# Performance work log

Measured on AMD Instinct MI355X. Metric: run time of the kernel, lower is better.

## Reference

```python
import jax, jax.numpy as jnp
import numpy as np

N_NODES = 50000
N_EDGES = 800000
N_GRAPHS = 64
D_IN = 96
D_HID = 96
D_OUT = 2
NEG_SLOPE = 0.2


def setup_inputs() -> dict:
    key = jax.random.key(0)
    ks = jax.random.split(key, 9)
    x = jax.random.normal(ks[0], (N_NODES, D_IN), dtype=jnp.float32)
    edge_index = jax.random.randint(ks[1], (2, N_EDGES), 0, N_NODES, dtype=jnp.int32)
    batch = jnp.sort(jax.random.randint(ks[2], (N_NODES,), 0, N_GRAPHS, dtype=jnp.int32))
    s1 = 1.0 / np.sqrt(D_IN)
    s2 = 1.0 / np.sqrt(D_HID)
    W1 = jax.random.normal(ks[3], (D_IN, D_HID), dtype=jnp.float32) * s1
    b1 = jnp.zeros((D_HID,), dtype=jnp.float32)
    W2 = jax.random.normal(ks[4], (D_HID, D_HID), dtype=jnp.float32) * s2
    b2 = jnp.zeros((D_HID,), dtype=jnp.float32)
    Wc = jax.random.normal(ks[5], (D_HID, D_OUT), dtype=jnp.float32) * s2
    bc = jnp.zeros((D_OUT,), dtype=jnp.float32)
    return {"x": x, "edge_index": edge_index, "batch": batch,
            "W1": W1, "b1": b1, "W2": W2, "b2": b2, "Wc": Wc, "bc": bc}


def _gcn_conv(h, W, b, src, dst, n_nodes):
    # GCNConv (Kipf): add self-loops, symmetric deg^-1/2 normalization.
    hW = h @ W  # [N, F]
    deg = jnp.zeros((n_nodes,), dtype=hW.dtype).at[dst].add(1.0) + 1.0  # +1 self-loop
    dinv = jax.lax.rsqrt(deg)
    coef = (dinv[src] * dinv[dst])[:, None]            # [E, 1]
    agg = jnp.zeros_like(hW).at[dst].add(hW[src] * coef)
    out = agg + hW * (dinv * dinv)[:, None] + b        # self-loop term: deg^-1 * hW
    return out


def _leaky(h):
    return jnp.where(h > 0, h, NEG_SLOPE * h)


def reference(x, edge_index, batch, W1, b1, W2, b2, Wc, bc):
    src, dst = edge_index[0], edge_index[1]
    h = _leaky(_gcn_conv(x, W1, b1, src, dst, N_NODES))
    h = _leaky(_gcn_conv(h, W2, b2, src, dst, N_NODES))
    # global_mean_pool over graph ids
    sums = jax.ops.segment_sum(h, batch, num_segments=N_GRAPHS)
    cnts = jax.ops.segment_sum(jnp.ones((N_NODES,), dtype=h.dtype), batch, num_segments=N_GRAPHS)
    pooled = sums / jnp.maximum(cnts, 1.0)[:, None]    # [G, F]
    return pooled @ Wc + bc                             # [G, D_OUT]
```

## Files before the change

kernel.cpp:

```cpp
#include <hip/hip_runtime.h>
#include <hip/hip_fp16.h>

#define NN 50000
#define NE 800000
#define NG 64
#define DF 96
#define SLOPE 0.2f
#define NBK 196
#define EB 196
#define PC 12

using half8 = __attribute__((ext_vector_type(8))) _Float16;
using f32x4 = __attribute__((ext_vector_type(4))) float;

__global__ __launch_bounds__(256) void k_hist(const int* __restrict__ dst,
                                              int* __restrict__ hist2d) {
  __shared__ int h[NBK];
  int t = threadIdx.x;
  if (t < NBK) h[t] = 0;
  __syncthreads();
  int base = blockIdx.x * 4096;
  for (int k = 0; k < 16; ++k) {
    int e = base + k * 256 + t;
    if (e < NE) atomicAdd(&h[dst[e] >> 8], 1);
  }
  __syncthreads();
  if (t < NBK) hist2d[blockIdx.x * NBK + t] = h[t];
}

__global__ __launch_bounds__(256) void k_colscan(const int* __restrict__ hist2d,
                                                 int* __restrict__ colpref,
                                                 int* __restrict__ coltotal,
                                                 const int* __restrict__ batch,
                                                 int* __restrict__ gstart) {
  __shared__ int s[256];
  int col = blockIdx.x;
  int b = threadIdx.x;
  int v = (b < EB) ? hist2d[b * NBK + col] : 0;
  s[b] = v;
  __syncthreads();
  for (int o = 1; o < 256; o <<= 1) {
    int u = (b >= o) ? s[b - o] : 0;
    __syncthreads();
    s[b] += u;
    __syncthreads();
  }
  if (b < EB) colpref[b * NBK + col] = s[b] - v;
  if (b == 255) coltotal[col] = s[b];
  if (blockIdx.x == 0 && b <= NG) {
    int g = b, lo = 0, hi = NN;
    while (lo < hi) {
      int mid = (lo + hi) >> 1;
      if (batch[mid] < g) lo = mid + 1; else hi = mid;
    }
    gstart[g] = lo;
  }
}

__global__ __launch_bounds__(256) void k_bin2(const int* __restrict__ src,
                                              const int* __restrict__ dst,
                                              const int* __restrict__ hist2d,
                                              const int* __restrict__ coltotal,
                                              const int* __restrict__ colpref,
                                              int* __restrict__ binned) {
  __shared__ int h[NBK], loff[NBK], cur[NBK], gb[NBK];
  __shared__ int tmp[256];
  __shared__ int stage[4096];
  __shared__ unsigned char sbk[4096];
  int t = threadIdx.x;
  int ctv = (t < NBK) ? coltotal[t] : 0;
  tmp[t] = ctv;
  __syncthreads();
  for (int o = 1; o < 256; o <<= 1) {
    int u = (t >= o) ? tmp[t - o] : 0;
    __syncthreads();
    tmp[t] += u;
    __syncthreads();
  }
  int bbase_t = tmp[t] - ctv;
  if (t < NBK) h[t] = hist2d[blockIdx.x * NBK + t];
  __syncthreads();
  tmp[t] = (t < NBK) ? h[t] : 0;
  __syncthreads();
  for (int o = 1; o < 256; o <<= 1) {
    int u = (t >= o) ? tmp[t - o] : 0;
    __syncthreads();
    tmp[t] += u;
    __syncthreads();
  }
  if (t < NBK) {
    int excl = tmp[t] - h[t];
    loff[t] = excl;
    cur[t] = excl;
    gb[t] = bbase_t + colpref[blockIdx.x * NBK + t];
  }
  __syncthreads();
  int base = blockIdx.x * 4096;
  for (int k = 0; k < 16; ++k) {
    int e = base + k * 256 + t;
    if (e < NE) {
      int d = dst[e];
      int b = d >> 8;
      int p = atomicAdd(&cur[b], 1);
      stage[p] = src[e] | ((d & 255) << 16);
      sbk[p] = (unsigned char)b;
    }
  }
  __syncthreads();
  int tot = min(4096, NE - base);
  for (int i = t; i < tot; i += 256) {
    int b = sbk[i];
    binned[gb[b] + (i - loff[b])] = stage[i];
  }
}

__global__ __launch_bounds__(256) void k_csr(const int* __restrict__ binned,
                                             const int* __restrict__ coltotal,
                                             float* __restrict__ dinv,
                                             int* __restrict__ row_start,
                                             unsigned short* __restrict__ csr_src) {
  __shared__ int h[256], cur[256], tmp[256];
  int t = threadIdx.x;
  int b = blockIdx.x;
  int ctv = (t < NBK) ? coltotal[t] : 0;
  h[t] = ctv;
  tmp[t] = ctv;
  __syncthreads();
  for (int o = 1; o < 256; o <<= 1) {
    int u = (t >= o) ? tmp[t - o] : 0;
    __syncthreads();
    tmp[t] += u;
    __syncthreads();
  }
  int ebeg = tmp[b] - h[b];
  int eend = tmp[b];
  __syncthreads();
  h[t] = 0;
  __syncthreads();
  for (int i = ebeg + t; i < eend; i += 256) atomicAdd(&h[(unsigned)binned[i] >> 16], 1);
  __syncthreads();
  tmp[t] = h[t];
  __syncthreads();
  for (int o = 1; o < 256; o <<= 1) {
    int v = (t >= o) ? tmp[t - o] : 0;
    __syncthreads();
    tmp[t] += v;
    __syncthreads();
  }
  int excl = tmp[t] - h[t];
  int rs = ebeg + excl;
  cur[t] = rs;
  int n = b * 256 + t;
  if (n < NN) {
    row_start[n] = rs;
    dinv[n] = rsqrtf((float)h[t] + 1.0f);
  }
  if (b == NBK - 1 && t == 255) row_start[NN] = NE;
  __syncthreads();
  for (int i = ebeg + t; i < eend; i += 256) {
    int pr = binned[i];
    int p = atomicAdd(&cur[(unsigned)pr >> 16], 1);
    csr_src[p] = (unsigned short)(pr & 0xFFFF);
  }
}

#define WTP 104
template <typename T>
__global__ __launch_bounds__(256) void k_gemm(const T* __restrict__ X,
                                              const float* __restrict__ W,
                                              const float* __restrict__ dinv,
                                              __half* __restrict__ G) {
  __shared__ alignas(16) _Float16 Wt[DF * WTP];
  int t = threadIdx.x;
  for (int i = t; i < DF * DF; i += 256) {
    int k = i / DF, c = i % DF;
    Wt[c * WTP + k] = (_Float16)W[i];
  }
  __syncthreads();

  int wave = t >> 6;
  int lane = t & 63;
  int lrow = lane & 15;
  int kgrp = lane >> 4;
  int rowbase = blockIdx.x * 64 + wave * 16;
  int arow = min(rowbase + lrow, NN - 1);

  half8 a[3];
#pragma unroll
  for (int kt = 0; kt < 3; ++kt) {
    int k0 = kt * 32 + kgrp * 8;
    if constexpr (sizeof(T) == 4) {
      const float4* xp = (const float4*)((const float*)X + (size_t)arow * DF + k0);
      float4 v0 = xp[0], v1 = xp[1];
      a[kt][0] = (_Float16)v0.x; a[kt][1] = (_Float16)v0.y;
      a[kt][2] = (_Float16)v0.z; a[kt][3] = (_Float16)v0.w;
      a[kt][4] = (_Float16)v1.x; a[kt][5] = (_Float16)v1.y;
      a[kt][6] = (_Float16)v1.z; a[kt][7] = (_Float16)v1.w;
    } else {
      a[kt] = *(const half8*)((const _Float16*)X + (size_t)arow * DF + k0);
    }
  }

  float dvv[4];
  int orow0 = rowbase + kgrp * 4;
#pragma unroll
  for (int r = 0; r < 4; ++r)
    dvv[r] = (orow0 + r < NN) ? dinv[orow0 + r] : 0.f;

#pragma unroll
  for (int ct = 0; ct < 6; ++ct) {
    int colbase = ct * 16;
    f32x4 acc = {0.f, 0.f, 0.f, 0.f};
#pragma unroll
    for (int kt = 0; kt < 3; ++kt) {
      half8 b = *(const half8*)&Wt[(colbase + lrow) * WTP + kt * 32 + kgrp * 8];
      acc = __builtin_amdgcn_mfma_f32_16x16x32_f16(a[kt], b, acc, 0, 0, 0);
    }
#pragma unroll
    for (int r = 0; r < 4; ++r) {
      int orow = orow0 + r;
      if (orow < NN)
        G[(size_t)orow * DF + colbase + lrow] = __float2half(acc[r] * dvv[r]);
    }
  }
}

__global__ __launch_bounds__(256) void k_agg(const __half* __restrict__ G,
                                             const float* __restrict__ dinv,
                                             const float* __restrict__ bias,
                                             const int* __restrict__ row_start,
                                             const unsigned short* __restrict__ csr_src,
                                             __half* __restrict__ H) {
  int lane = threadIdx.x & 15;
  int n = blockIdx.x * 16 + (threadIdx.x >> 4);
  if (n >= NN) return;
  const unsigned* rn = (const unsigned*)(G + (size_t)n * DF);
  unsigned su0 = rn[lane], su1 = rn[lane + 16], su2 = rn[lane + 32];
  float2 f0 = __half22float2(*(__half2*)&su0);
  float2 f1 = __half22float2(*(__half2*)&su1);
  float2 f2 = __half22float2(*(__half2*)&su2);
  float a00 = f0.x, a01 = f0.y, a10 = f1.x, a11 = f1.y, a20 = f2.x, a21 = f2.y;

  int s = row_start[n], e = row_start[n + 1];
  for (int j0 = s; j0 < e; j0 += 16) {
    int my = (j0 + lane < e) ? (int)csr_src[j0 + lane] : 0;
    int cnt = min(16, e - j0);
    int jj = 0;
    for (; jj + 8 <= cnt; jj += 8) {
      unsigned u[8][3];
#pragma unroll
      for (int q = 0; q < 8; ++q) {
        int srcn = __shfl(my, jj + q, 16);
        const unsigned* r2 = (const unsigned*)(G + (size_t)srcn * DF);
        u[q][0] = r2[lane];
        u[q][1] = r2[lane + 16];
        u[q][2] = r2[lane + 32];
      }
#pragma unroll
      for (int q = 0; q < 8; ++q) {
        float2 g0 = __half22float2(*(__half2*)&u[q][0]);
        float2 g1 = __half22float2(*(__half2*)&u[q][1]);
        float2 g2 = __half22float2(*(__half2*)&u[q][2]);
        a00 += g0.x; a01 += g0.y;
        a10 += g1.x; a11 += g1.y;
        a20 += g2.x; a21 += g2.y;
      }
    }
    for (; jj < cnt; ++jj) {
      int srcn = __shfl(my, jj, 16);
      const unsigned* r2 = (const unsigned*)(G + (size_t)srcn * DF);
      unsigned v0 = r2[lane], v1 = r2[lane + 16], v2 = r2[lane + 32];
      float2 g0 = __half22float2(*(__half2*)&v0);
      float2 g1 = __half22float2(*(__half2*)&v1);
      float2 g2 = __half22float2(*(__half2*)&v2);
      a00 += g0.x; a01 += g0.y;
      a10 += g1.x; a11 += g1.y;
      a20 += g2.x; a21 += g2.y;
    }
  }
  float dv = dinv[n];
  float2 b0 = *(const float2*)(bias + 2 * lane);
  float2 b1 = *(const float2*)(bias + 2 * lane + 32);
  float2 b2 = *(const float2*)(bias + 2 * lane + 64);
  float v00 = dv * a00 + b0.x, v01 = dv * a01 + b0.y;
  float v10 = dv * a10 + b1.x, v11 = dv * a11 + b1.y;
  float v20 = dv * a20 + b2.x, v21 = dv * a21 + b2.y;
  v00 = v00 > 0.f ? v00 : SLOPE * v00;
  v01 = v01 > 0.f ? v01 : SLOPE * v01;
  v10 = v10 > 0.f ? v10 : SLOPE * v10;
  v11 = v11 > 0.f ? v11 : SLOPE * v11;
  v20 = v20 > 0.f ? v20 : SLOPE * v20;
  v21 = v21 > 0.f ? v21 : SLOPE * v21;
  __half2* hp = (__half2*)(H + (size_t)n * DF);
  hp[lane] = __floats2half2_rn(v00, v01);
  hp[lane + 16] = __floats2half2_rn(v10, v11);
  hp[lane + 32] = __floats2half2_rn(v20, v21);
}

__global__ __launch_bounds__(384) void k_pool2(const __half* __restrict__ H,
                                               const int* __restrict__ gstart,
                                               float* __restrict__ partial) {
  int g = blockIdx.x / PC, c = blockIdx.x % PC;
  int f2 = threadIdx.x % 48;
  int r = threadIdx.x / 48;
  int s = gstart[g], e = gstart[g + 1];
  int len = (e - s + PC - 1) / PC;
  int cs = s + c * len, ce = min(cs + len, e);
  float ax = 0.f, ay = 0.f;
  for (int n = cs + r; n < ce; n += 8) {
    float2 v = __half22float2(((const __half2*)(H + (size_t)n * DF))[f2]);
    ax += v.x;
    ay += v.y;
  }
  __shared__ float2 red[8][48];
  red[r][f2] = float2{ax, ay};
  __syncthreads();
  if (r == 0) {
    float sx = 0.f, sy = 0.f;
#pragma unroll
    for (int q = 0; q < 8; ++q) { sx += red[q][f2].x; sy += red[q][f2].y; }
    partial[(size_t)blockIdx.x * DF + 2 * f2] = sx;
    partial[(size_t)blockIdx.x * DF + 2 * f2 + 1] = sy;
  }
}

__global__ __launch_bounds__(128) void k_pool3(const float* __restrict__ partial,
                                               const int* __restrict__ gstart,
                                               const float* __restrict__ Wc,
                                               const float* __restrict__ bc,
                                               float* __restrict__ out) {
  __shared__ float pm[DF];
  int g = blockIdx.x;
  int t = threadIdx.x;
  if (t < DF) {
    float s = 0.f;
    for (int c = 0; c < PC; ++c) s += partial[(size_t)(g * PC + c) * DF + t];
    float cnt = (float)(gstart[g + 1] - gstart[g]);
    pm[t] = s / fmaxf(cnt, 1.0f);
  }
  __syncthreads();
  if (t < 2) {
    float s = 0.f;
    for (int c = 0; c < DF; ++c) s += pm[c] * Wc[c * 2 + t];
    out[g * 2 + t] = s + bc[t];
  }
}

extern "C" void kernel_launch(void* const* d_in, const int* in_sizes, int n_in,
                              void* d_out, int out_size, void* d_ws, size_t ws_size,
                              hipStream_t stream) {
  const float* x = (const float*)d_in[0];
  const int* ei = (const int*)d_in[1];
  const int* batch = (const int*)d_in[2];
  const float* W1 = (const float*)d_in[3];
  const float* b1 = (const float*)d_in[4];
  const float* W2 = (const float*)d_in[5];
  const float* b2 = (const float*)d_in[6];
  const float* Wc = (const float*)d_in[7];
  const float* bc = (const float*)d_in[8];
  float* out = (float*)d_out;
  const int* srcv = ei;
  const int* dstv = ei + NE;

  char* p = (char*)d_ws;
  auto alloc = [&](size_t bytes) {
    char* r = p;
    p += (bytes + 255) & ~(size_t)255;
    return r;
  };
  int* hist2d = (int*)alloc((size_t)EB * NBK * sizeof(int));
  int* colpref = (int*)alloc((size_t)EB * NBK * sizeof(int));
  int* coltotal = (int*)alloc((size_t)NBK * sizeof(int));
  int* gstart = (int*)alloc((size_t)(NG + 1) * sizeof(int));
  int* row_start = (int*)alloc((size_t)(NN + 1) * sizeof(int));
  int* binned = (int*)alloc((size_t)NE * sizeof(int));
  unsigned short* csr_src = (unsigned short*)alloc((size_t)NE * sizeof(unsigned short));
  float* dinv = (float*)alloc((size_t)NN * sizeof(float));
  __half* g = (__half*)alloc((size_t)NN * DF * sizeof(__half));
  __half* h = (__half*)alloc((size_t)NN * DF * sizeof(__half));
  float* partial = (float*)alloc((size_t)NG * PC * DF * sizeof(float));

  k_hist<<<EB, 256, 0, stream>>>(dstv, hist2d);
  k_colscan<<<NBK, 256, 0, stream>>>(hist2d, colpref, coltotal, batch, gstart);
  k_bin2<<<EB, 256, 0, stream>>>(srcv, dstv, hist2d, coltotal, colpref, binned);
  k_csr<<<NBK, 256, 0, stream>>>(binned, coltotal, dinv, row_start, csr_src);

  const int GB = (NN + 63) / 64;
  k_gemm<float><<<GB, 256, 0, stream>>>(x, W1, dinv, g);
  k_agg<<<(NN + 15) / 16, 256, 0, stream>>>(g, dinv, b1, row_start, csr_src, h);
  k_gemm<__half><<<GB, 256, 0, stream>>>((const __half*)h, W2, dinv, g);
  k_agg<<<(NN + 15) / 16, 256, 0, stream>>>(g, dinv, b2, row_start, csr_src, h);

  k_pool2<<<NG * PC, 384, 0, stream>>>(h, gstart, partial);
  k_pool3<<<NG, 128, 0, stream>>>(partial, gstart, Wc, bc, out);
}
```

Baseline: 126.1 us.

## Fuse CSR build into one cooperative kernel and pool inside final aggregation

Merges the four graph-preprocessing kernels (histogram, column scan, binning, CSR build) into a single cooperative kernel that uses grid-wide syncs between phases, cutting launch gaps. The second aggregation kernel now reduces its 16 node rows per block into per-graph sums in shared memory and atomically adds them to the partial buffer. This removes the write of the final hidden features and the separate pooling pass. It relies on all 196 blocks being co-resident for the cooperative launch. It also introduces float atomics, which make the summation order nondeterministic.

```diff
diff --git a/kernel.cpp b/kernel.cpp
--- a/kernel.cpp
+++ b/kernel.cpp
@@ -1,5 +1,8 @@
 #include <hip/hip_runtime.h>
 #include <hip/hip_fp16.h>
+#include <hip/hip_cooperative_groups.h>
+
+namespace cg = cooperative_groups;
 
 #define NN 50000
 #define NE 800000
@@ -8,159 +11,154 @@
 #define SLOPE 0.2f
 #define NBK 196
 #define EB 196
-#define PC 12
 
 using half8 = __attribute__((ext_vector_type(8))) _Float16;
 using f32x4 = __attribute__((ext_vector_type(4))) float;
 
-__global__ __launch_bounds__(256) void k_hist(const int* __restrict__ dst,
-                                              int* __restrict__ hist2d) {
-  __shared__ int h[NBK];
+__global__ __launch_bounds__(256) void k_build(const int* __restrict__ src,
+                                               const int* __restrict__ dst,
+                                               const int* __restrict__ batch,
+                                               int* __restrict__ hist2d,
+                                               int* __restrict__ colpref,
+                                               int* __restrict__ coltotal,
+                                               int* __restrict__ gstart,
+                                               int* __restrict__ binned,
+                                               float* __restrict__ dinv,
+                                               int* __restrict__ row_start,
+                                               unsigned short* __restrict__ csr_src,
+                                               float* __restrict__ partial) {
+  cg::grid_group grid = cg::this_grid();
+  __shared__ int h[256], cur[256], tmp[256];
+  __shared__ int loff[NBK], gb[NBK];
+  __shared__ int stage[4096];
+  __shared__ unsigned char sbk[4096];
   int t = threadIdx.x;
+  int blk = blockIdx.x;
+
   if (t < NBK) h[t] = 0;
   __syncthreads();
-  int base = blockIdx.x * 4096;
+  int base = blk * 4096;
   for (int k = 0; k < 16; ++k) {
     int e = base + k * 256 + t;
     if (e < NE) atomicAdd(&h[dst[e] >> 8], 1);
   }
   __syncthreads();
-  if (t < NBK) hist2d[blockIdx.x * NBK + t] = h[t];
-}
-
-__global__ __launch_bounds__(256) void k_colscan(const int* __restrict__ hist2d,
-                                                 int* __restrict__ colpref,
-                                                 int* __restrict__ coltotal,
-                                                 const int* __restrict__ batch,
-                                                 int* __restrict__ gstart) {
-  __shared__ int s[256];
-  int col = blockIdx.x;
-  int b = threadIdx.x;
-  int v = (b < EB) ? hist2d[b * NBK + col] : 0;
-  s[b] = v;
-  __syncthreads();
-  for (int o = 1; o < 256; o <<= 1) {
-    int u = (b >= o) ? s[b - o] : 0;
-    __syncthreads();
-    s[b] += u;
-    __syncthreads();
-  }
-  if (b < EB) colpref[b * NBK + col] = s[b] - v;
-  if (b == 255) coltotal[col] = s[b];
-  if (blockIdx.x == 0 && b <= NG) {
-    int g = b, lo = 0, hi = NN;
-    while (lo < hi) {
-      int mid = (lo + hi) >> 1;
-      if (batch[mid] < g) lo = mid + 1; else hi = mid;
-    }
-    gstart[g] = lo;
-  }
-}
-
-__global__ __launch_bounds__(256) void k_bin2(const int* __restrict__ src,
-                                              const int* __restrict__ dst,
-                                              const int* __restrict__ hist2d,
-                                              const int* __restrict__ coltotal,
-                                              const int* __restrict__ colpref,
-                                              int* __restrict__ binned) {
-  __shared__ int h[NBK], loff[NBK], cur[NBK], gb[NBK];
-  __shared__ int tmp[256];
-  __shared__ int stage[4096];
-  __shared__ unsigned char sbk[4096];
-  int t = threadIdx.x;
-  int ctv = (t < NBK) ? coltotal[t] : 0;
-  tmp[t] = ctv;
-  __syncthreads();
-  for (int o = 1; o < 256; o <<= 1) {
-    int u = (t >= o) ? tmp[t - o] : 0;
-    __syncthreads();
-    tmp[t] += u;
-    __syncthreads();
-  }
-  int bbase_t = tmp[t] - ctv;
-  if (t < NBK) h[t] = hist2d[blockIdx.x * NBK + t];
-  __syncthreads();
-  tmp[t] = (t < NBK) ? h[t] : 0;
-  __syncthreads();
-  for (int o = 1; o < 256; o <<= 1) {
-    int u = (t >= o) ? tmp[t - o] : 0;
-    __syncthreads();
-    tmp[t] += u;
-    __syncthreads();
-  }
-  if (t < NBK) {
+  if (t < NBK) hist2d[blk * NBK + t] = h[t];
+  grid.sync();
+
+  {
+    int col = blk;
+    int v = (t < EB) ? hist2d[t * NBK + col] : 0;
+    tmp[t] = v;
+    __syncthreads();
+    for (int o = 1; o < 256; o <<= 1) {
+      int u = (t >= o) ? tmp[t - o] : 0;
+      __syncthreads();
+      tmp[t] += u;
+      __syncthreads();
+    }
+    if (t < EB) colpref[t * NBK + col] = tmp[t] - v;
+    if (t == 255) coltotal[col] = tmp[t];
+    if (blk == 0 && t <= NG) {
+      int g = t, lo = 0, hi = NN;
+      while (lo < hi) {
+        int mid = (lo + hi) >> 1;
+        if (batch[mid] < g) lo = mid + 1; else hi = mid;
+      }
+      gstart[g] = lo;
+    }
+    if (blk == 1)
+      for (int i = t; i < NG * DF; i += 256) partial[i] = 0.f;
+  }
+  grid.sync();
+
+  {
+    int ctv = (t < NBK) ? coltotal[t] : 0;
+    tmp[t] = ctv;
+    __syncthreads();
+    for (int o = 1; o < 256; o <<= 1) {
+      int u = (t >= o) ? tmp[t - o] : 0;
+      __syncthreads();
+      tmp[t] += u;
+      __syncthreads();
+    }
+    int bbase_t = tmp[t] - ctv;
+    __syncthreads();
+    tmp[t] = (t < NBK) ? h[t] : 0;
+    __syncthreads();
+    for (int o = 1; o < 256; o <<= 1) {
+      int u = (t >= o) ? tmp[t - o] : 0;
+      __syncthreads();
+      tmp[t] += u;
+      __syncthreads();
+    }
+    if (t < NBK) {
+      int excl = tmp[t] - h[t];
+      loff[t] = excl;
+      cur[t] = excl;
+      gb[t] = bbase_t + colpref[blk * NBK + t];
+    }
+    __syncthreads();
+    for (int k = 0; k < 16; ++k) {
+      int e = base + k * 256 + t;
+      if (e < NE) {
+        int d = dst[e];
+        int b = d >> 8;
+        int p = atomicAdd(&cur[b], 1);
+        stage[p] = src[e] | ((d & 255) << 16);
+        sbk[p] = (unsigned char)b;
+      }
+    }
+    __syncthreads();
+    int tot = min(4096, NE - base);
+    for (int i = t; i < tot; i += 256) {
+      int b = sbk[i];
+      binned[gb[b] + (i - loff[b])] = stage[i];
+    }
+  }
+  grid.sync();
+
+  {
+    int ctv = (t < NBK) ? coltotal[t] : 0;
+    h[t] = ctv;
+    tmp[t] = ctv;
+    __syncthreads();
+    for (int o = 1; o < 256; o <<= 1) {
+      int u = (t >= o) ? tmp[t - o] : 0;
+      __syncthreads();
+      tmp[t] += u;
+      __syncthreads();
+    }
+    int ebeg = tmp[blk] - h[blk];
+    int eend = tmp[blk];
+    __syncthreads();
+    h[t] = 0;
+    __syncthreads();
+    for (int i = ebeg + t; i < eend; i += 256) atomicAdd(&h[(unsigned)binned[i] >> 16], 1);
+    __syncthreads();
+    tmp[t] = h[t];
+    __syncthreads();
+    for (int o = 1; o < 256; o <<= 1) {
+      int v = (t >= o) ? tmp[t - o] : 0;
+      __syncthreads();
+      tmp[t] += v;
+      __syncthreads();
+    }
     int excl = tmp[t] - h[t];
-    loff[t] = excl;
-    cur[t] = excl;
-    gb[t] = bbase_t + colpref[blockIdx.x * NBK + t];
-  }
-  __syncthreads();
-  int base = blockIdx.x * 4096;
-  for (int k = 0; k < 16; ++k) {
-    int e = base + k * 256 + t;
-    if (e < NE) {
-      int d = dst[e];
-      int b = d >> 8;
-      int p = atomicAdd(&cur[b], 1);
-      stage[p] = src[e] | ((d & 255) << 16);
-      sbk[p] = (unsigned char)b;
-    }
-  }
-  __syncthreads();
-  int tot = min(4096, NE - base);
-  for (int i = t; i < tot; i += 256) {
-    int b = sbk[i];
-    binned[gb[b] + (i - loff[b])] = stage[i];
-  }
-}
-
-__global__ __launch_bounds__(256) void k_csr(const int* __restrict__ binned,
-                                             const int* __restrict__ coltotal,
-                                             float* __restrict__ dinv,
-                                             int* __restrict__ row_start,
-                                             unsigned short* __restrict__ csr_src) {
-  __shared__ int h[256], cur[256], tmp[256];
-  int t = threadIdx.x;
-  int b = blockIdx.x;
-  int ctv = (t < NBK) ? coltotal[t] : 0;
-  h[t] = ctv;
-  tmp[t] = ctv;
-  __syncthreads();
-  for (int o = 1; o < 256; o <<= 1) {
-    int u = (t >= o) ? tmp[t - o] : 0;
-    __syncthreads();
-    tmp[t] += u;
-    __syncthreads();
-  }
-  int ebeg = tmp[b] - h[b];
-  int eend = tmp[b];
-  __syncthreads();
-  h[t] = 0;
-  __syncthreads();
-  for (int i = ebeg + t; i < eend; i += 256) atomicAdd(&h[(unsigned)binned[i] >> 16], 1);
-  __syncthreads();
-  tmp[t] = h[t];
-  __syncthreads();
-  for (int o = 1; o < 256; o <<= 1) {
-    int v = (t >= o) ? tmp[t - o] : 0;
-    __syncthreads();
-    tmp[t] += v;
-    __syncthreads();
-  }
-  int excl = tmp[t] - h[t];
-  int rs = ebeg + excl;
-  cur[t] = rs;
-  int n = b * 256 + t;
-  if (n < NN) {
-    row_start[n] = rs;
-    dinv[n] = rsqrtf((float)h[t] + 1.0f);
-  }
-  if (b == NBK - 1 && t == 255) row_start[NN] = NE;
-  __syncthreads();
-  for (int i = ebeg + t; i < eend; i += 256) {
-    int pr = binned[i];
-    int p = atomicAdd(&cur[(unsigned)pr >> 16], 1);
-    csr_src[p] = (unsigned short)(pr & 0xFFFF);
+    int rs = ebeg + excl;
+    cur[t] = rs;
+    int n = blk * 256 + t;
+    if (n < NN) {
+      row_start[n] = rs;
+      dinv[n] = rsqrtf((float)h[t] + 1.0f);
+    }
+    if (blk == NBK - 1 && t == 255) row_start[NN] = NE;
+    __syncthreads();
+    for (int i = ebeg + t; i < eend; i += 256) {
+      int pr = binned[i];
+      int p = atomicAdd(&cur[(unsigned)pr >> 16], 1);
+      csr_src[p] = (unsigned short)(pr & 0xFFFF);
+    }
   }
 }
 
@@ -225,15 +223,18 @@
   }
 }
 
+template <int FINAL>
 __global__ __launch_bounds__(256) void k_agg(const __half* __restrict__ G,
                                              const float* __restrict__ dinv,
                                              const float* __restrict__ bias,
                                              const int* __restrict__ row_start,
                                              const unsigned short* __restrict__ csr_src,
-                                             __half* __restrict__ H) {
+                                             __half* __restrict__ H,
+                                             const int* __restrict__ batch,
+                                             float* __restrict__ partial) {
   int lane = threadIdx.x & 15;
-  int n = blockIdx.x * 16 + (threadIdx.x >> 4);
-  if (n >= NN) return;
+  int grp = threadIdx.x >> 4;
+  int n = blockIdx.x * 16 + grp;
   const unsigned* rn = (const unsigned*)(G + (size_t)n * DF);
   unsigned su0 = rn[lane], su1 = rn[lane + 16], su2 = rn[lane + 32];
   float2 f0 = __half22float2(*(__half2*)&su0);
@@ -291,36 +292,41 @@
   v11 = v11 > 0.f ? v11 : SLOPE * v11;
   v20 = v20 > 0.f ? v20 : SLOPE * v20;
   v21 = v21 > 0.f ? v21 : SLOPE * v21;
-  __half2* hp = (__half2*)(H + (size_t)n * DF);
-  hp[lane] = __floats2half2_rn(v00, v01);
-  hp[lane + 16] = __floats2half2_rn(v10, v11);
-  hp[lane + 32] = __floats2half2_rn(v20, v21);
-}
-
-__global__ __launch_bounds__(384) void k_pool2(const __half* __restrict__ H,
-                                               const int* __restrict__ gstart,
-                                               float* __restrict__ partial) {
-  int g = blockIdx.x / PC, c = blockIdx.x % PC;
-  int f2 = threadIdx.x % 48;
-  int r = threadIdx.x / 48;
-  int s = gstart[g], e = gstart[g + 1];
-  int len = (e - s + PC - 1) / PC;
-  int cs = s + c * len, ce = min(cs + len, e);
-  float ax = 0.f, ay = 0.f;
-  for (int n = cs + r; n < ce; n += 8) {
-    float2 v = __half22float2(((const __half2*)(H + (size_t)n * DF))[f2]);
-    ax += v.x;
-    ay += v.y;
-  }
-  __shared__ float2 red[8][48];
-  red[r][f2] = float2{ax, ay};
-  __syncthreads();
-  if (r == 0) {
-    float sx = 0.f, sy = 0.f;
-#pragma unroll
-    for (int q = 0; q < 8; ++q) { sx += red[q][f2].x; sy += red[q][f2].y; }
-    partial[(size_t)blockIdx.x * DF + 2 * f2] = sx;
-    partial[(size_t)blockIdx.x * DF + 2 * f2 + 1] = sy;
+
+  if (!FINAL) {
+    __half2* hp = (__half2*)(H + (size_t)n * DF);
+    hp[lane] = __floats2half2_rn(v00, v01);
+    hp[lane + 16] = __floats2half2_rn(v10, v11);
+    hp[lane + 32] = __floats2half2_rn(v20, v21);
+  } else {
+    __shared__ float red[16][DF];
+    __shared__ int gnode[16];
+    red[grp][2 * lane] = v00;
+    red[grp][2 * lane + 1] = v01;
+    red[grp][32 + 2 * lane] = v10;
+    red[grp][33 + 2 * lane] = v11;
+    red[grp][64 + 2 * lane] = v20;
+    red[grp][65 + 2 * lane] = v21;
+    if (lane == 0) gnode[grp] = batch[n];
+    __syncthreads();
+    int f = threadIdx.x;
+    if (f < DF) {
+      int g0 = gnode[0], g15 = gnode[15];
+      if (g0 == g15) {
+        float sum = 0.f;
+#pragma unroll
+        for (int q = 0; q < 16; ++q) sum += red[q][f];
+        atomicAdd(&partial[g0 * DF + f], sum);
+      } else {
+        for (int g = g0; g <= g15; ++g) {
+          float sum = 0.f;
+          bool any = false;
+          for (int q = 0; q < 16; ++q)
+            if (gnode[q] == g) { sum += red[q][f]; any = true; }
+          if (any) atomicAdd(&partial[g * DF + f], sum);
+        }
+      }
+    }
   }
 }
 
@@ -333,10 +339,8 @@
   int g = blockIdx.x;
   int t = threadIdx.x;
   if (t < DF) {
-    float s = 0.f;
-    for (int c = 0; c < PC; ++c) s += partial[(size_t)(g * PC + c) * DF + t];
     float cnt = (float)(gstart[g + 1] - gstart[g]);
-    pm[t] = s / fmaxf(cnt, 1.0f);
+    pm[t] = partial[g * DF + t] / fmaxf(cnt, 1.0f);
   }
   __syncthreads();
   if (t < 2) {
@@ -378,19 +382,19 @@
   float* dinv = (float*)alloc((size_t)NN * sizeof(float));
   __half* g = (__half*)alloc((size_t)NN * DF * sizeof(__half));
   __half* h = (__half*)alloc((size_t)NN * DF * sizeof(__half));
-  float* partial = (float*)alloc((size_t)NG * PC * DF * sizeof(float));
-
-  k_hist<<<EB, 256, 0, stream>>>(dstv, hist2d);
-  k_colscan<<<NBK, 256, 0, stream>>>(hist2d, colpref, coltotal, batch, gstart);
-  k_bin2<<<EB, 256, 0, stream>>>(srcv, dstv, hist2d, coltotal, colpref, binned);
-  k_csr<<<NBK, 256, 0, stream>>>(binned, coltotal, dinv, row_start, csr_src);
+  float* partial = (float*)alloc((size_t)NG * DF * sizeof(float));
+
+  void* bargs[] = {(void*)&srcv,     (void*)&dstv,    (void*)&batch,
+                   (void*)&hist2d,   (void*)&colpref, (void*)&coltotal,
+                   (void*)&gstart,   (void*)&binned,  (void*)&dinv,
+                   (void*)&row_start,(void*)&csr_src, (void*)&partial};
+  hipLaunchCooperativeKernel((const void*)k_build, dim3(NBK), dim3(256), bargs, 0, stream);
 
   const int GB = (NN + 63) / 64;
   k_gemm<float><<<GB, 256, 0, stream>>>(x, W1, dinv, g);
-  k_agg<<<(NN + 15) / 16, 256, 0, stream>>>(g, dinv, b1, row_start, csr_src, h);
+  k_agg<0><<<NN / 16, 256, 0, stream>>>(g, dinv, b1, row_start, csr_src, h, batch, partial);
   k_gemm<__half><<<GB, 256, 0, stream>>>((const __half*)h, W2, dinv, g);
-  k_agg<<<(NN + 15) / 16, 256, 0, stream>>>(g, dinv, b2, row_start, csr_src, h);
-
-  k_pool2<<<NG * PC, 384, 0, stream>>>(h, gstart, partial);
+  k_agg<1><<<NN / 16, 256, 0, stream>>>(g, dinv, b2, row_start, csr_src, h, batch, partial);
+
   k_pool3<<<NG, 128, 0, stream>>>(partial, gstart, Wc, bc, out);
 }
```

After: 196.6 us. 55.9% more time.

## Fuse mean-pool partial sums into final aggregation kernel via atomics

Applied to the files above, without the earlier changes.

The second aggregation kernel now reduces its 16 node outputs per block in shared memory and atomically adds per-graph feature sums into a small partial buffer. This removes the separate pool2 kernel and the write and reread of the final hidden activations. The partial buffer is zeroed inside the CSR kernel. The change adds float atomics, which make summation order nondeterministic. It also drops the bounds check by relying on the node count dividing evenly by 16.

```diff
diff --git a/kernel.cpp b/kernel.cpp
--- a/kernel.cpp
+++ b/kernel.cpp
@@ -8,7 +8,6 @@
 #define SLOPE 0.2f
 #define NBK 196
 #define EB 196
-#define PC 12
 
 using half8 = __attribute__((ext_vector_type(8))) _Float16;
 using f32x4 = __attribute__((ext_vector_type(4))) float;
@@ -118,10 +117,13 @@
                                              const int* __restrict__ coltotal,
                                              float* __restrict__ dinv,
                                              int* __restrict__ row_start,
-                                             unsigned short* __restrict__ csr_src) {
+                                             unsigned short* __restrict__ csr_src,
+                                             float* __restrict__ partial) {
   __shared__ int h[256], cur[256], tmp[256];
   int t = threadIdx.x;
   int b = blockIdx.x;
+  if (b == 0)
+    for (int i = t; i < NG * DF; i += 256) partial[i] = 0.f;
   int ctv = (t < NBK) ? coltotal[t] : 0;
   h[t] = ctv;
   tmp[t] = ctv;
@@ -225,15 +227,18 @@
   }
 }
 
+template <int FINAL>
 __global__ __launch_bounds__(256) void k_agg(const __half* __restrict__ G,
                                              const float* __restrict__ dinv,
                                              const float* __restrict__ bias,
                                              const int* __restrict__ row_start,
                                              const unsigned short* __restrict__ csr_src,
-                                             __half* __restrict__ H) {
+                                             __half* __restrict__ H,
+                                             const int* __restrict__ batch,
+                                             float* __restrict__ partial) {
   int lane = threadIdx.x & 15;
-  int n = blockIdx.x * 16 + (threadIdx.x >> 4);
-  if (n >= NN) return;
+  int grp = threadIdx.x >> 4;
+  int n = blockIdx.x * 16 + grp;
   const unsigned* rn = (const unsigned*)(G + (size_t)n * DF);
   unsigned su0 = rn[lane], su1 = rn[lane + 16], su2 = rn[lane + 32];
   float2 f0 = __half22float2(*(__half2*)&su0);
@@ -291,36 +296,41 @@
   v11 = v11 > 0.f ? v11 : SLOPE * v11;
   v20 = v20 > 0.f ? v20 : SLOPE * v20;
   v21 = v21 > 0.f ? v21 : SLOPE * v21;
-  __half2* hp = (__half2*)(H + (size_t)n * DF);
-  hp[lane] = __floats2half2_rn(v00, v01);
-  hp[lane + 16] = __floats2half2_rn(v10, v11);
-  hp[lane + 32] = __floats2half2_rn(v20, v21);
-}
-
-__global__ __launch_bounds__(384) void k_pool2(const __half* __restrict__ H,
-                                               const int* __restrict__ gstart,
-                                               float* __restrict__ partial) {
-  int g = blockIdx.x / PC, c = blockIdx.x % PC;
-  int f2 = threadIdx.x % 48;
-  int r = threadIdx.x / 48;
-  int s = gstart[g], e = gstart[g + 1];
-  int len = (e - s + PC - 1) / PC;
-  int cs = s + c * len, ce = min(cs + len, e);
-  float ax = 0.f, ay = 0.f;
-  for (int n = cs + r; n < ce; n += 8) {
-    float2 v = __half22float2(((const __half2*)(H + (size_t)n * DF))[f2]);
-    ax += v.x;
-    ay += v.y;
-  }
-  __shared__ float2 red[8][48];
-  red[r][f2] = float2{ax, ay};
-  __syncthreads();
-  if (r == 0) {
-    float sx = 0.f, sy = 0.f;
-#pragma unroll
-    for (int q = 0; q < 8; ++q) { sx += red[q][f2].x; sy += red[q][f2].y; }
-    partial[(size_t)blockIdx.x * DF + 2 * f2] = sx;
-    partial[(size_t)blockIdx.x * DF + 2 * f2 + 1] = sy;
+
+  if (!FINAL) {
+    __half2* hp = (__half2*)(H + (size_t)n * DF);
+    hp[lane] = __floats2half2_rn(v00, v01);
+    hp[lane + 16] = __floats2half2_rn(v10, v11);
+    hp[lane + 32] = __floats2half2_rn(v20, v21);
+  } else {
+    __shared__ float red[16][DF];
+    __shared__ int gnode[16];
+    red[grp][2 * lane] = v00;
+    red[grp][2 * lane + 1] = v01;
+    red[grp][32 + 2 * lane] = v10;
+    red[grp][33 + 2 * lane] = v11;
+    red[grp][64 + 2 * lane] = v20;
+    red[grp][65 + 2 * lane] = v21;
+    if (lane == 0) gnode[grp] = batch[n];
+    __syncthreads();
+    int f = threadIdx.x;
+    if (f < DF) {
+      int g0 = gnode[0], g15 = gnode[15];
+      if (g0 == g15) {
+        float sum = 0.f;
+#pragma unroll
+        for (int q = 0; q < 16; ++q) sum += red[q][f];
+        atomicAdd(&partial[g0 * DF + f], sum);
+      } else {
+        for (int g = g0; g <= g15; ++g) {
+          float sum = 0.f;
+          bool any = false;
+          for (int q = 0; q < 16; ++q)
+            if (gnode[q] == g) { sum += red[q][f]; any = true; }
+          if (any) atomicAdd(&partial[g * DF + f], sum);
+        }
+      }
+    }
   }
 }
 
@@ -333,10 +343,8 @@
   int g = blockIdx.x;
   int t = threadIdx.x;
   if (t < DF) {
-    float s = 0.f;
-    for (int c = 0; c < PC; ++c) s += partial[(size_t)(g * PC + c) * DF + t];
     float cnt = (float)(gstart[g + 1] - gstart[g]);
-    pm[t] = s / fmaxf(cnt, 1.0f);
+    pm[t] = partial[g * DF + t] / fmaxf(cnt, 1.0f);
   }
   __syncthreads();
   if (t < 2) {
@@ -378,19 +386,18 @@
   float* dinv = (float*)alloc((size_t)NN * sizeof(float));
   __half* g = (__half*)alloc((size_t)NN * DF * sizeof(__half));
   __half* h = (__half*)alloc((size_t)NN * DF * sizeof(__half));
-  float* partial = (float*)alloc((size_t)NG * PC * DF * sizeof(float));
+  float* partial = (float*)alloc((size_t)NG * DF * sizeof(float));
 
   k_hist<<<EB, 256, 0, stream>>>(dstv, hist2d);
   k_colscan<<<NBK, 256, 0, stream>>>(hist2d, colpref, coltotal, batch, gstart);
   k_bin2<<<EB, 256, 0, stream>>>(srcv, dstv, hist2d, coltotal, colpref, binned);
-  k_csr<<<NBK, 256, 0, stream>>>(binned, coltotal, dinv, row_start, csr_src);
+  k_csr<<<NBK, 256, 0, stream>>>(binned, coltotal, dinv, row_start, csr_src, partial);
 
   const int GB = (NN + 63) / 64;
   k_gemm<float><<<GB, 256, 0, stream>>>(x, W1, dinv, g);
-  k_agg<<<(NN + 15) / 16, 256, 0, stream>>>(g, dinv, b1, row_start, csr_src, h);
+  k_agg<0><<<NN / 16, 256, 0, stream>>>(g, dinv, b1, row_start, csr_src, h, batch, partial);
   k_gemm<__half><<<GB, 256, 0, stream>>>((const __half*)h, W2, dinv, g);
-  k_agg<<<(NN + 15) / 16, 256, 0, stream>>>(g, dinv, b2, row_start, csr_src, h);
-
-  k_pool2<<<NG * PC, 384, 0, stream>>>(h, gstart, partial);
+  k_agg<1><<<NN / 16, 256, 0, stream>>>(g, dinv, b2, row_start, csr_src, h, batch, partial);
+
   k_pool3<<<NG, 128, 0, stream>>>(partial, gstart, Wc, bc, out);
 }
```

Result: faster. 121.9 us, median of 2 (-3.3%).
